# Performance work log

Hardware: AMD Instinct MI355X
Metric: run time of the kernel (lower is better)

## Reference

```python
import jax, jax.numpy as jnp
import numpy as np

B, T, N, D, E, H = 4, 512, 512, 1024, 1024, 16
HD = D // H
EPS = 1e-6

def _ln(h):
    mu = jnp.mean(h, axis=-1, keepdims=True)
    var = jnp.mean(jnp.square(h - mu), axis=-1, keepdims=True)
    return (h - mu) / jnp.sqrt(var + EPS)

def setup_inputs() -> dict:
    key = jax.random.key(0)
    ks = jax.random.split(key, 20)
    s = 0.02
    return {
        "x1": jax.random.normal(ks[0], (B, T, D), jnp.float32),
        "x2": jax.random.normal(ks[1], (B, T, D), jnp.float32),
        "x3": jax.random.normal(ks[2], (B, T, D), jnp.float32),
        "xf": jax.random.normal(ks[3], (B, N, D), jnp.float32),
        "emb": jax.random.normal(ks[4], (B, E), jnp.float32),
        "key_padding_mask": jnp.zeros((B, N), dtype=bool),
        # AdaLN params (branch-stacked), weights stored (in,out)
        "adaln_w": jax.random.normal(ks[5], (3, E, 2 * D), jnp.float32) * s,
        "adaln_b": jnp.zeros((3, 2 * D), jnp.float32),
        "xf_adaln_w": jax.random.normal(ks[6], (E, 2 * D), jnp.float32) * s,
        "xf_adaln_b": jnp.zeros((2 * D,), jnp.float32),
        "q_w": jax.random.normal(ks[7], (3, D, D), jnp.float32) * s,
        "q_b": jnp.zeros((3, D), jnp.float32),
        "k_w": jax.random.normal(ks[8], (D, D), jnp.float32) * s,
        "k_b": jnp.zeros((D,), jnp.float32),
        "v_w": jax.random.normal(ks[9], (D, D), jnp.float32) * s,
        "v_b": jnp.zeros((D,), jnp.float32),
        "out_w": jax.random.normal(ks[10], (3, D, D), jnp.float32) * s,
        "out_b": jnp.zeros((3, D), jnp.float32),
    }

def reference(x1, x2, x3, xf, emb, key_padding_mask,
              adaln_w, adaln_b, xf_adaln_w, xf_adaln_b,
              q_w, q_b, k_w, k_b, v_w, v_b, out_w, out_b):
    se = jax.nn.silu(emb)  # (B,E)
    xs = [x1, x2, x3]
    Qs = []
    for i in range(3):
        eo = se @ adaln_w[i] + adaln_b[i]            # (B,2D)
        scale, shift = jnp.split(eo, 2, axis=-1)
        h = _ln(xs[i]) * (1.0 + scale[:, None]) + shift[:, None]
        Qs.append((h @ q_w[i] + q_b[i]).reshape(B, T, H, HD))
    Q = jnp.concatenate(Qs, axis=1)                  # (B,3T,H,HD)

    eo = se @ xf_adaln_w + xf_adaln_b
    scale, shift = jnp.split(eo, 2, axis=-1)
    xfn = _ln(xf) * (1.0 + scale[:, None]) + shift[:, None]
    K = (xfn @ k_w + k_b).reshape(B, N, H, HD)
    V = (xfn @ v_w + v_b).reshape(B, N, H, HD)

    logits = jnp.einsum('bthd,bnhd->bhtn', Q, K) / jnp.sqrt(jnp.float32(HD))
    logits = jnp.where(key_padding_mask[:, None, None, :], -jnp.inf, logits)
    attn = jax.nn.softmax(logits, axis=-1)           # dropout is identity (eval)
    out = jnp.einsum('bhtn,bnhd->bthd', attn, V).reshape(B, 3 * T, D)

    out1 = out[:, :T] @ out_w[0] + out_b[0]
    out2 = out[:, T:2 * T] @ out_w[1] + out_b[1]
    out3 = out[:, 2 * T:3 * T] @ out_w[2] + out_b[2]
    return (out1, out2, out3)
```

## Files before the change

### kernel.cpp

```cpp
#include <hip/hip_runtime.h>
#include <hip/hip_bf16.h>
#include <stdint.h>

#define BB 4
#define TSEQ 512
#define NSEQ 512
#define DD 1024
#define EE 1024
#define HH 16
#define HD 64

typedef __attribute__((ext_vector_type(8))) short bf16x8;
typedef __attribute__((ext_vector_type(4))) float f32x4;

__device__ __forceinline__ unsigned short f2bf(float f) {
    union { float f; uint32_t u; } v; v.f = f;
    uint32_t u = v.u;
    uint32_t r = (u + 0x7fffu + ((u >> 16) & 1u)) >> 16;
    return (unsigned short)r;
}

__device__ __forceinline__ uint32_t pkbf(float a, float b) {
    __hip_bfloat162 t = __float22bfloat162_rn(float2{a, b});
    return *(uint32_t*)&t;
}

#define GLD16(gp, lp)                                                          \
    __builtin_amdgcn_global_load_lds(                                          \
        (const __attribute__((address_space(1))) unsigned int*)(gp),           \
        (__attribute__((address_space(3))) unsigned int*)(lp), 16, 0, 0)

__global__ __launch_bounds__(256) void tw_all_kernel(
    const float* __restrict__ q_w, const float* __restrict__ k_w,
    const float* __restrict__ v_w, const float* __restrict__ out_w,
    unsigned short* __restrict__ qwt, unsigned short* __restrict__ kwt,
    unsigned short* __restrict__ vwt, unsigned short* __restrict__ owt)
{
    __shared__ __align__(16) unsigned short Ts[64 * 72];
    int k0 = blockIdx.x * 64, n0 = blockIdx.y * 64;
    int z = blockIdx.z;
    const float* in; unsigned short* out;
    if (z < 3)       { in = q_w + (size_t)z * DD * DD;         out = qwt + (size_t)z * DD * DD; }
    else if (z == 3) { in = k_w;                               out = kwt; }
    else if (z == 4) { in = v_w;                               out = vwt; }
    else             { in = out_w + (size_t)(z - 5) * DD * DD; out = owt + (size_t)(z - 5) * DD * DD; }
    int tid = threadIdx.x;
    int r = tid >> 2, c0 = (tid & 3) * 16;
#pragma unroll
    for (int i = 0; i < 4; i++) {
        float4 v = *(const float4*)(in + (size_t)(k0 + r) * DD + n0 + c0 + i * 4);
        Ts[(c0 + i * 4 + 0) * 72 + r] = f2bf(v.x);
        Ts[(c0 + i * 4 + 1) * 72 + r] = f2bf(v.y);
        Ts[(c0 + i * 4 + 2) * 72 + r] = f2bf(v.z);
        Ts[(c0 + i * 4 + 3) * 72 + r] = f2bf(v.w);
    }
    __syncthreads();
#pragma unroll
    for (int i = 0; i < 2; i++) {
        int idx = i * 256 + tid;
        int row = idx >> 3, ko = (idx & 7) * 8;
        *(uint4*)(out + (size_t)(n0 + row) * DD + k0 + ko) =
            *(const uint4*)(Ts + row * 72 + ko);
    }
}

__global__ __launch_bounds__(256) void adaln_kernel(
    const float* __restrict__ emb,
    const float* __restrict__ adaln_w, const float* __restrict__ adaln_b,
    const float* __restrict__ xf_w, const float* __restrict__ xf_b,
    float* __restrict__ scaleB, float* __restrict__ shiftB)
{
    __shared__ __align__(16) float seT[EE][4];
    __shared__ float buf[128 * 33];
    int tid = threadIdx.x;
    int chunk = blockIdx.x, j = blockIdx.y;
#pragma unroll
    for (int b = 0; b < 4; b++) {
        float4 e4 = ((const float4*)(emb + (size_t)b * EE))[tid];
        seT[tid * 4 + 0][b] = e4.x / (1.f + __expf(-e4.x));
        seT[tid * 4 + 1][b] = e4.y / (1.f + __expf(-e4.y));
        seT[tid * 4 + 2][b] = e4.z / (1.f + __expf(-e4.z));
        seT[tid * 4 + 3][b] = e4.w / (1.f + __expf(-e4.w));
    }
    __syncthreads();
    const float* W    = (j < 3) ? (adaln_w + (size_t)j * EE * 2 * DD) : xf_w;
    const float* bias = (j < 3) ? (adaln_b + (size_t)j * 2 * DD) : xf_b;
    int eg = tid >> 3, cg = tid & 7;
    int c0 = chunk * 32 + cg * 4;
    const float* Wp = W + (size_t)(eg * 32) * (2 * DD) + c0;
    float4 a0 = {0,0,0,0}, a1 = {0,0,0,0}, a2 = {0,0,0,0}, a3 = {0,0,0,0};
#pragma unroll 8
    for (int e = 0; e < 32; e++) {
        float4 w = *(const float4*)(Wp + (size_t)e * (2 * DD));
        float4 s = *(const float4*)&seT[eg * 32 + e][0];
        a0.x += s.x * w.x; a0.y += s.x * w.y; a0.z += s.x * w.z; a0.w += s.x * w.w;
        a1.x += s.y * w.x; a1.y += s.y * w.y; a1.z += s.y * w.z; a1.w += s.y * w.w;
        a2.x += s.z * w.x; a2.y += s.z * w.y; a2.z += s.z * w.z; a2.w += s.z * w.w;
        a3.x += s.w * w.x; a3.y += s.w * w.y; a3.z += s.w * w.z; a3.w += s.w * w.w;
    }
    float accs[4][4] = {{a0.x,a0.y,a0.z,a0.w},{a1.x,a1.y,a1.z,a1.w},
                        {a2.x,a2.y,a2.z,a2.w},{a3.x,a3.y,a3.z,a3.w}};
#pragma unroll
    for (int b = 0; b < 4; b++)
#pragma unroll
        for (int i = 0; i < 4; i++)
            buf[(b * 32 + cg * 4 + i) * 33 + eg] = accs[b][i];
    __syncthreads();
    if (tid < 128) {
        int b = tid >> 5, cl = tid & 31;
        float s = 0.f;
#pragma unroll 8
        for (int e = 0; e < 32; e++) s += buf[(b * 32 + cl) * 33 + e];
        int c = chunk * 32 + cl;
        float v = s + bias[c];
        if (c < DD) scaleB[(size_t)(j * 4 + b) * DD + c] = v;
        else        shiftB[(size_t)(j * 4 + b) * DD + (c - DD)] = v;
    }
}

__global__ __launch_bounds__(256) void ln_mod_kernel(
    const float* __restrict__ x1, const float* __restrict__ x2,
    const float* __restrict__ x3, const float* __restrict__ xf,
    const float* __restrict__ scaleB, const float* __restrict__ shiftB,
    unsigned short* __restrict__ hq, unsigned short* __restrict__ hx)
{
    __shared__ float rs[4], rq[4];
    int row = blockIdx.x, tid = threadIdx.x;
    const float* src; unsigned short* dst; int sb;
    if (row < 6144) {
        int b = row / 1536, t3 = row % 1536;
        int br = t3 >> 9, t = t3 & 511;
        const float* xs = (br == 0) ? x1 : ((br == 1) ? x2 : x3);
        src = xs + ((size_t)b * TSEQ + t) * DD;
        dst = hq + (size_t)row * DD;
        sb = br * 4 + b;
    } else {
        int idx = row - 6144;
        src = xf + (size_t)idx * DD;
        dst = hx + (size_t)idx * DD;
        sb = 12 + (idx >> 9);
    }
    float4 x = ((const float4*)src)[tid];
    float s = x.x + x.y + x.z + x.w;
    float q = x.x * x.x + x.y * x.y + x.z * x.z + x.w * x.w;
    for (int o = 1; o < 64; o <<= 1) { s += __shfl_xor(s, o, 64); q += __shfl_xor(q, o, 64); }
    int lane = tid & 63, wid = tid >> 6;
    if (lane == 0) { rs[wid] = s; rq[wid] = q; }
    __syncthreads();
    float S = rs[0] + rs[1] + rs[2] + rs[3];
    float Q = rq[0] + rq[1] + rq[2] + rq[3];
    float mu = S * (1.f / DD);
    float var = Q * (1.f / DD) - mu * mu;
    float rstd = rsqrtf(var + 1e-6f);
    float4 sc = ((const float4*)(scaleB + (size_t)sb * DD))[tid];
    float4 sh = ((const float4*)(shiftB + (size_t)sb * DD))[tid];
    ushort4 o;
    o.x = f2bf((x.x - mu) * rstd * (1.f + sc.x) + sh.x);
    o.y = f2bf((x.y - mu) * rstd * (1.f + sc.y) + sh.y);
    o.z = f2bf((x.z - mu) * rstd * (1.f + sc.z) + sh.z);
    o.w = f2bf((x.w - mu) * rstd * (1.f + sc.w) + sh.w);
    ((ushort4*)dst)[tid] = o;
}

__device__ __forceinline__ void gemm_core128(
    const unsigned short* __restrict__ A, const unsigned short* __restrict__ W,
    int m0, int n0, unsigned short* As, unsigned short* Bs,
    int tid, f32x4 acc[4][4])
{
    int lane = tid & 63, wid = tid >> 6;
    int fm = lane & 15, quad = lane >> 4;
    int wm = wid >> 1, wn = wid & 1;
    int sr = tid >> 3;
    int sc = tid & 7;
    int gko = (sc ^ (sr & 7)) * 8;
    const unsigned short* Ap = A + (size_t)(m0 + sr) * DD + gko;
    const unsigned short* Wp = W + (size_t)(n0 + sr) * DD + gko;
    unsigned short* la = As + tid * 8;
    unsigned short* lb = Bs + tid * 8;
    int f7 = fm & 7;
    for (int k0 = 0; k0 < DD; k0 += 64) {
#pragma unroll
        for (int i = 0; i < 4; i++)
            GLD16(Ap + (size_t)(32 * i) * DD + k0, la + i * 2048);
#pragma unroll
        for (int i = 0; i < 4; i++)
            GLD16(Wp + (size_t)(32 * i) * DD + k0, lb + i * 2048);
        __syncthreads();
#pragma unroll
        for (int kh = 0; kh < 2; kh++) {
            int sq = ((quad + 4 * kh) ^ f7) * 8;
            bf16x8 af[4], bfr[4];
#pragma unroll
            for (int mt = 0; mt < 4; mt++)
                af[mt] = *(const bf16x8*)(As + (wm * 64 + mt * 16 + fm) * 64 + sq);
#pragma unroll
            for (int nt = 0; nt < 4; nt++)
                bfr[nt] = *(const bf16x8*)(Bs + (wn * 64 + nt * 16 + fm) * 64 + sq);
#pragma unroll
            for (int mt = 0; mt < 4; mt++)
#pragma unroll
                for (int nt = 0; nt < 4; nt++)
                    acc[mt][nt] = __builtin_amdgcn_mfma_f32_16x16x32_bf16(af[mt], bfr[nt], acc[mt][nt], 0, 0, 0);
        }
        __syncthreads();
    }
}

__global__ __launch_bounds__(256) void qkv_gemm(
    const unsigned short* __restrict__ hq, const unsigned short* __restrict__ hx,
    const unsigned short* __restrict__ qwt, const unsigned short* __restrict__ kwt,
    const unsigned short* __restrict__ vwt,
    const float* __restrict__ q_b, const float* __restrict__ k_b,
    const float* __restrict__ v_b,
    unsigned short* __restrict__ Qpk, unsigned short* __restrict__ Kpk,
    unsigned short* __restrict__ Vpk)
{
    __shared__ __align__(16) unsigned short As[128 * 64];
    __shared__ __align__(16) unsigned short Bs[128 * 64];
    int id = blockIdx.x;
    int ty = id % 80, n0 = (id / 80) * 128;
    const unsigned short *A, *W; const float* bias; int mode, m0;
    if (ty < 48) {
        m0 = ty * 128;
        int br = (m0 % 1536) >> 9;
        A = hq; W = qwt + (size_t)br * DD * DD; bias = q_b + (size_t)br * DD; mode = 0;
    } else if (ty < 64) {
        m0 = (ty - 48) * 128; A = hx; W = kwt; bias = k_b; mode = 1;
    } else {
        m0 = (ty - 64) * 128; A = hx; W = vwt; bias = v_b; mode = 2;
    }
    int tid = threadIdx.x, lane = tid & 63, wid = tid >> 6;
    int fm = lane & 15, quad = lane >> 4;
    int wm = wid >> 1, wn = wid & 1;
    f32x4 z = {0.f, 0.f, 0.f, 0.f};
    f32x4 acc[4][4];
#pragma unroll
    for (int mt = 0; mt < 4; mt++)
#pragma unroll
        for (int nt = 0; nt < 4; nt++) acc[mt][nt] = z;
    gemm_core128(A, W, m0, n0, As, Bs, tid, acc);
#pragma unroll
    for (int mt = 0; mt < 4; mt++) {
#pragma unroll
        for (int nt = 0; nt < 4; nt++) {
            int c = n0 + wn * 64 + nt * 16 + fm;
            float bv = bias[c];
            int r0 = m0 + wm * 64 + mt * 16 + quad * 4;
            int h = c >> 6;
            if (mode == 0) {
                int b = r0 / 1536, t3 = r0 % 1536;
                int kk = (c >> 5) & 1, o = c & 31;
                size_t base = ((((size_t)(b * HH + h) * 2 + kk) * 1536) + t3) * 32 + o;
#pragma unroll
                for (int reg = 0; reg < 4; reg++)
                    Qpk[base + (size_t)reg * 32] = f2bf((acc[mt][nt][reg] + bv) * 0.125f);
            } else if (mode == 1) {
                int b = r0 >> 9, n = r0 & 511;
                int kk = (c >> 5) & 1, o = c & 31;
                size_t base = ((((size_t)(b * HH + h) * 2 + kk) * 512) + n) * 32 + o;
#pragma unroll
                for (int reg = 0; reg < 4; reg++)
                    Kpk[base + (size_t)reg * 32] = f2bf(acc[mt][nt][reg] + bv);
            } else {
                int b = r0 >> 9, n = r0 & 511;
                int hd = c & 63, cv = n >> 5, ko = n & 31;
                ushort4 st;
                st.x = f2bf(acc[mt][nt][0] + bv);
                st.y = f2bf(acc[mt][nt][1] + bv);
                st.z = f2bf(acc[mt][nt][2] + bv);
                st.w = f2bf(acc[mt][nt][3] + bv);
                *(ushort4*)(Vpk + ((((size_t)(b * HH + h) * 16 + cv) * 64) + hd) * 32 + ko) = st;
            }
        }
    }
}

__global__ __launch_bounds__(256) void out_gemm(
    const unsigned short* __restrict__ Ain, const unsigned short* __restrict__ owt,
    const float* __restrict__ out_b, float* __restrict__ outp)
{
    __shared__ __align__(16) unsigned short As[128 * 64];
    __shared__ __align__(16) unsigned short Bs[128 * 64];
    int id = blockIdx.x;
    int m0 = (id % 48) * 128, n0 = (id / 48) * 128;
    int br = (m0 % 1536) >> 9;
    const unsigned short* W = owt + (size_t)br * DD * DD;
    const float* bias = out_b + (size_t)br * DD;
    int tid = threadIdx.x, lane = tid & 63, wid = tid >> 6;
    int fm = lane & 15, quad = lane >> 4;
    int wm = wid >> 1, wn = wid & 1;
    f32x4 z = {0.f, 0.f, 0.f, 0.f};
    f32x4 acc[4][4];
#pragma unroll
    for (int mt = 0; mt < 4; mt++)
#pragma unroll
        for (int nt = 0; nt < 4; nt++) acc[mt][nt] = z;
    gemm_core128(Ain, W, m0, n0, As, Bs, tid, acc);
#pragma unroll
    for (int mt = 0; mt < 4; mt++) {
#pragma unroll
        for (int nt = 0; nt < 4; nt++) {
            int c = n0 + wn * 64 + nt * 16 + fm;
            float bv = bias[c];
            int r0 = m0 + wm * 64 + mt * 16 + quad * 4;
            int b = r0 / 1536, t3 = r0 % 1536, t = t3 & 511;
#pragma unroll
            for (int reg = 0; reg < 4; reg++)
                outp[(size_t)br * (BB * TSEQ * DD) + (size_t)b * (TSEQ * DD)
                     + (size_t)(t + reg) * DD + c] = acc[mt][nt][reg] + bv;
        }
    }
}

__global__ __launch_bounds__(256, 4) void attn_kernel(
    const unsigned short* __restrict__ Qpk,
    const unsigned short* __restrict__ Kpk,
    const unsigned short* __restrict__ Vpk,
    const unsigned char* __restrict__ mask,
    unsigned short* __restrict__ attn)
{
    __shared__ __align__(16) unsigned short P[32 * 520];
    __shared__ float redsum[128];
    int orig = blockIdx.x;
    int wg = (orig & 7) * 384 + (orig >> 3);
    int bh = wg / 48, b = bh >> 4, h = bh & 15;
    int m0 = (wg % 48) * 32;
    int tid = threadIdx.x, lane = tid & 63, w = tid >> 6;
    int fm = lane & 15, quad = lane >> 4;

    const unsigned char* mp = mask + (size_t)b * NSEQ + w * 128;
    unsigned long long mw0 = __ballot(mp[lane] != 0);
    unsigned long long mw1 = __ballot(mp[64 + lane] != 0);

    f32x4 acc[8][2];
#pragma unroll
    for (int mt = 0; mt < 8; mt++) {
        unsigned long long word = (mt >= 4) ? mw1 : mw0;
        int kb = (mt * 16 + quad * 4) & 63;
        f32x4 ini;
#pragma unroll
        for (int reg = 0; reg < 4; reg++)
            ini[reg] = ((word >> (kb + reg)) & 1ull) ? -1e30f : 0.f;
        acc[mt][0] = ini; acc[mt][1] = ini;
    }
    const unsigned short* Kbase = Kpk + (size_t)bh * 2 * 512 * 32 + quad * 8;
    const unsigned short* Qbase = Qpk + (size_t)bh * 2 * 1536 * 32 + quad * 8;
    const unsigned short* Vbase = Vpk + (size_t)bh * 16 * 64 * 32 + (size_t)(w * 16 + fm) * 32 + quad * 8;
#pragma unroll
    for (int kk = 0; kk < 2; kk++) {
        bf16x8 bq0 = *(const bf16x8*)(Qbase + (size_t)(kk * 1536 + m0 + fm) * 32);
        bf16x8 bq1 = *(const bf16x8*)(Qbase + (size_t)(kk * 1536 + m0 + 16 + fm) * 32);
#pragma unroll
        for (int mt = 0; mt < 8; mt++) {
            bf16x8 ak = *(const bf16x8*)(Kbase + (size_t)(kk * 512 + w * 128 + mt * 16 + fm) * 32);
            acc[mt][0] = __builtin_amdgcn_mfma_f32_16x16x32_bf16(ak, bq0, acc[mt][0], 0, 0, 0);
            acc[mt][1] = __builtin_amdgcn_mfma_f32_16x16x32_bf16(ak, bq1, acc[mt][1], 0, 0, 0);
        }
    }

    bf16x8 vpre[8];
#pragma unroll
    for (int kk = 0; kk < 8; kk++)
        vpre[kk] = *(const bf16x8*)(Vbase + (size_t)kk * 64 * 32);

    float s0 = 0.f, s1 = 0.f;
#pragma unroll
    for (int mt = 0; mt < 8; mt++) {
        float e00 = __expf(acc[mt][0][0]);
        float e01 = __expf(acc[mt][0][1]);
        float e02 = __expf(acc[mt][0][2]);
        float e03 = __expf(acc[mt][0][3]);
        float e10 = __expf(acc[mt][1][0]);
        float e11 = __expf(acc[mt][1][1]);
        float e12 = __expf(acc[mt][1][2]);
        float e13 = __expf(acc[mt][1][3]);
        s0 += (e00 + e01) + (e02 + e03);
        s1 += (e10 + e11) + (e12 + e13);
        uint2 p0, p1;
        p0.x = pkbf(e00, e01); p0.y = pkbf(e02, e03);
        p1.x = pkbf(e10, e11); p1.y = pkbf(e12, e13);
        int kb = w * 128 + mt * 16 + quad * 4;
        *(uint2*)(P + (size_t)fm * 520 + kb) = p0;
        *(uint2*)(P + (size_t)(16 + fm) * 520 + kb) = p1;
    }
    s0 += __shfl_xor(s0, 16, 64); s0 += __shfl_xor(s0, 32, 64);
    s1 += __shfl_xor(s1, 16, 64); s1 += __shfl_xor(s1, 32, 64);
    if (quad == 0) { redsum[w * 32 + fm] = s0; redsum[w * 32 + 16 + fm] = s1; }
    __syncthreads();

    float inv0 = 1.f / (redsum[fm] + redsum[32 + fm] + redsum[64 + fm] + redsum[96 + fm]);
    float inv1 = 1.f / (redsum[16 + fm] + redsum[48 + fm] + redsum[80 + fm] + redsum[112 + fm]);
    bf16x8 vrest[8];
#pragma unroll
    for (int kk = 0; kk < 8; kk++)
        vrest[kk] = *(const bf16x8*)(Vbase + (size_t)(8 + kk) * 64 * 32);
    f32x4 z = {0.f, 0.f, 0.f, 0.f};
    f32x4 o0 = z, o1 = z;
    const unsigned short* Pp0 = P + (size_t)fm * 520 + quad * 8;
    const unsigned short* Pp1 = P + (size_t)(16 + fm) * 520 + quad * 8;
#pragma unroll
    for (int kk = 0; kk < 8; kk++) {
        bf16x8 p0 = *(const bf16x8*)(Pp0 + kk * 32);
        bf16x8 p1 = *(const bf16x8*)(Pp1 + kk * 32);
        o0 = __builtin_amdgcn_mfma_f32_16x16x32_bf16(vpre[kk], p0, o0, 0, 0, 0);
        o1 = __builtin_amdgcn_mfma_f32_16x16x32_bf16(vpre[kk], p1, o1, 0, 0, 0);
    }
#pragma unroll
    for (int kk = 0; kk < 8; kk++) {
        bf16x8 p0 = *(const bf16x8*)(Pp0 + (8 + kk) * 32);
        bf16x8 p1 = *(const bf16x8*)(Pp1 + (8 + kk) * 32);
        o0 = __builtin_amdgcn_mfma_f32_16x16x32_bf16(vrest[kk], p0, o0, 0, 0, 0);
        o1 = __builtin_amdgcn_mfma_f32_16x16x32_bf16(vrest[kk], p1, o1, 0, 0, 0);
    }
    ushort4 r0, r1;
    r0.x = f2bf(o0[0] * inv0); r0.y = f2bf(o0[1] * inv0);
    r0.z = f2bf(o0[2] * inv0); r0.w = f2bf(o0[3] * inv0);
    r1.x = f2bf(o1[0] * inv1); r1.y = f2bf(o1[1] * inv1);
    r1.z = f2bf(o1[2] * inv1); r1.w = f2bf(o1[3] * inv1);
    *(ushort4*)(attn + ((size_t)(b * 1536 + m0 + fm)) * DD + h * HD + w * 16 + quad * 4) = r0;
    *(ushort4*)(attn + ((size_t)(b * 1536 + m0 + 16 + fm)) * DD + h * HD + w * 16 + quad * 4) = r1;
}

extern "C" void kernel_launch(void* const* d_in, const int* in_sizes, int n_in,
                              void* d_out, int out_size, void* d_ws, size_t ws_size,
                              hipStream_t stream)
{
    const float* x1   = (const float*)d_in[0];
    const float* x2   = (const float*)d_in[1];
    const float* x3   = (const float*)d_in[2];
    const float* xf   = (const float*)d_in[3];
    const float* emb  = (const float*)d_in[4];
    const unsigned char* mask = (const unsigned char*)d_in[5];
    const float* adaln_w = (const float*)d_in[6];
    const float* adaln_b = (const float*)d_in[7];
    const float* xf_w = (const float*)d_in[8];
    const float* xf_b = (const float*)d_in[9];
    const float* q_w  = (const float*)d_in[10];
    const float* q_b  = (const float*)d_in[11];
    const float* k_w  = (const float*)d_in[12];
    const float* k_b  = (const float*)d_in[13];
    const float* v_w  = (const float*)d_in[14];
    const float* v_b  = (const float*)d_in[15];
    const float* out_w = (const float*)d_in[16];
    const float* out_b = (const float*)d_in[17];

    char* ws = (char*)d_ws;
    float* scaleB        = (float*)(ws + 0);
    float* shiftB        = (float*)(ws + 65536);
    unsigned short* hq   = (unsigned short*)(ws + 131072);
    unsigned short* hx   = (unsigned short*)(ws + 12713984);
    unsigned short* Qpk  = (unsigned short*)(ws + 16908288);
    unsigned short* Kpk  = (unsigned short*)(ws + 29491200);
    unsigned short* Vpk  = (unsigned short*)(ws + 33685504);
    unsigned short* qwt  = (unsigned short*)(ws + 37879808);
    unsigned short* kwt  = (unsigned short*)(ws + 44171264);
    unsigned short* vwt  = (unsigned short*)(ws + 46268416);
    unsigned short* owt  = (unsigned short*)(ws + 48365568);

    tw_all_kernel<<<dim3(16, 16, 8), 256, 0, stream>>>(q_w, k_w, v_w, out_w,
                                                       qwt, kwt, vwt, owt);
    adaln_kernel<<<dim3(64, 4), 256, 0, stream>>>(emb, adaln_w, adaln_b, xf_w, xf_b,
                                                  scaleB, shiftB);
    ln_mod_kernel<<<8192, 256, 0, stream>>>(x1, x2, x3, xf, scaleB, shiftB, hq, hx);
    qkv_gemm<<<640, 256, 0, stream>>>(hq, hx, qwt, kwt, vwt, q_b, k_b, v_b,
                                      Qpk, Kpk, Vpk);
    attn_kernel<<<3072, 256, 0, stream>>>(Qpk, Kpk, Vpk, mask, hq);
    out_gemm<<<384, 256, 0, stream>>>(hq, owt, out_b, (float*)d_out);
}
```

Baseline: 259.7 us.

## Double-buffer LDS tiles in GEMM core to overlap global loads with MFMA

Converts the shared GEMM core used by the QKV and output projections into a two-stage software pipeline. The next K-slice is loaded asynchronously into a second LDS buffer while the current slice is consumed by MFMAs, with explicit vmcnt waits and raw barriers in place of __syncthreads. This aims to hide global-to-LDS latency but doubles LDS use per block to 64KB, which may reduce occupancy.

```diff
diff --git a/kernel.cpp b/kernel.cpp
--- a/kernel.cpp
+++ b/kernel.cpp
@@ -162,7 +162,7 @@
     ((ushort4*)dst)[tid] = o;
 }
 
-__device__ __forceinline__ void gemm_core128(
+__device__ __forceinline__ void gemm_core128_db(
     const unsigned short* __restrict__ A, const unsigned short* __restrict__ W,
     int m0, int n0, unsigned short* As, unsigned short* Bs,
     int tid, f32x4 acc[4][4])
@@ -175,34 +175,53 @@
     int gko = (sc ^ (sr & 7)) * 8;
     const unsigned short* Ap = A + (size_t)(m0 + sr) * DD + gko;
     const unsigned short* Wp = W + (size_t)(n0 + sr) * DD + gko;
-    unsigned short* la = As + tid * 8;
-    unsigned short* lb = Bs + tid * 8;
     int f7 = fm & 7;
-    for (int k0 = 0; k0 < DD; k0 += 64) {
-#pragma unroll
-        for (int i = 0; i < 4; i++)
-            GLD16(Ap + (size_t)(32 * i) * DD + k0, la + i * 2048);
-#pragma unroll
-        for (int i = 0; i < 4; i++)
-            GLD16(Wp + (size_t)(32 * i) * DD + k0, lb + i * 2048);
-        __syncthreads();
+
+    {
+        unsigned short* la = As + tid * 8;
+        unsigned short* lb = Bs + tid * 8;
+#pragma unroll
+        for (int i = 0; i < 4; i++) GLD16(Ap + (size_t)(32 * i) * DD, la + i * 2048);
+#pragma unroll
+        for (int i = 0; i < 4; i++) GLD16(Wp + (size_t)(32 * i) * DD, lb + i * 2048);
+    }
+
+    for (int t = 0; t < 16; t++) {
+        int cur = t & 1;
+        if (t < 15) {
+            unsigned short* na = As + (cur ^ 1) * 8192 + tid * 8;
+            unsigned short* nb = Bs + (cur ^ 1) * 8192 + tid * 8;
+            int k0 = (t + 1) * 64;
+#pragma unroll
+            for (int i = 0; i < 4; i++) GLD16(Ap + (size_t)(32 * i) * DD + k0, na + i * 2048);
+#pragma unroll
+            for (int i = 0; i < 4; i++) GLD16(Wp + (size_t)(32 * i) * DD + k0, nb + i * 2048);
+            asm volatile("s_waitcnt vmcnt(8)" ::: "memory");
+        } else {
+            asm volatile("s_waitcnt vmcnt(0)" ::: "memory");
+        }
+        __builtin_amdgcn_s_barrier();
+        __builtin_amdgcn_sched_barrier(0);
+        const unsigned short* Ab = As + cur * 8192;
+        const unsigned short* Bb = Bs + cur * 8192;
 #pragma unroll
         for (int kh = 0; kh < 2; kh++) {
             int sq = ((quad + 4 * kh) ^ f7) * 8;
             bf16x8 af[4], bfr[4];
 #pragma unroll
             for (int mt = 0; mt < 4; mt++)
-                af[mt] = *(const bf16x8*)(As + (wm * 64 + mt * 16 + fm) * 64 + sq);
+                af[mt] = *(const bf16x8*)(Ab + (wm * 64 + mt * 16 + fm) * 64 + sq);
 #pragma unroll
             for (int nt = 0; nt < 4; nt++)
-                bfr[nt] = *(const bf16x8*)(Bs + (wn * 64 + nt * 16 + fm) * 64 + sq);
+                bfr[nt] = *(const bf16x8*)(Bb + (wn * 64 + nt * 16 + fm) * 64 + sq);
 #pragma unroll
             for (int mt = 0; mt < 4; mt++)
 #pragma unroll
                 for (int nt = 0; nt < 4; nt++)
                     acc[mt][nt] = __builtin_amdgcn_mfma_f32_16x16x32_bf16(af[mt], bfr[nt], acc[mt][nt], 0, 0, 0);
         }
-        __syncthreads();
+        __builtin_amdgcn_s_barrier();
+        __builtin_amdgcn_sched_barrier(0);
     }
 }
 
@@ -215,8 +234,8 @@
     unsigned short* __restrict__ Qpk, unsigned short* __restrict__ Kpk,
     unsigned short* __restrict__ Vpk)
 {
-    __shared__ __align__(16) unsigned short As[128 * 64];
-    __shared__ __align__(16) unsigned short Bs[128 * 64];
+    __shared__ __align__(16) unsigned short As[2 * 128 * 64];
+    __shared__ __align__(16) unsigned short Bs[2 * 128 * 64];
     int id = blockIdx.x;
     int ty = id % 80, n0 = (id / 80) * 128;
     const unsigned short *A, *W; const float* bias; int mode, m0;
@@ -238,7 +257,7 @@
     for (int mt = 0; mt < 4; mt++)
 #pragma unroll
         for (int nt = 0; nt < 4; nt++) acc[mt][nt] = z;
-    gemm_core128(A, W, m0, n0, As, Bs, tid, acc);
+    gemm_core128_db(A, W, m0, n0, As, Bs, tid, acc);
 #pragma unroll
     for (int mt = 0; mt < 4; mt++) {
 #pragma unroll
@@ -279,8 +298,8 @@
     const unsigned short* __restrict__ Ain, const unsigned short* __restrict__ owt,
     const float* __restrict__ out_b, float* __restrict__ outp)
 {
-    __shared__ __align__(16) unsigned short As[128 * 64];
-    __shared__ __align__(16) unsigned short Bs[128 * 64];
+    __shared__ __align__(16) unsigned short As[2 * 128 * 64];
+    __shared__ __align__(16) unsigned short Bs[2 * 128 * 64];
     int id = blockIdx.x;
     int m0 = (id % 48) * 128, n0 = (id / 48) * 128;
     int br = (m0 % 1536) >> 9;
@@ -295,7 +314,7 @@
     for (int mt = 0; mt < 4; mt++)
 #pragma unroll
         for (int nt = 0; nt < 4; nt++) acc[mt][nt] = z;
-    gemm_core128(Ain, W, m0, n0, As, Bs, tid, acc);
+    gemm_core128_db(Ain, W, m0, n0, As, Bs, tid, acc);
 #pragma unroll
     for (int mt = 0; mt < 4; mt++) {
 #pragma unroll
```

New measurement: 260.0 us. No clear change (+0.1%).
